# Performance work log

Measured on AMD Instinct MI355X. Metric: run time of the kernel, lower is better.

## Reference

```python
import jax, jax.numpy as jnp
import numpy as np

N_HEADS = 16
D_EMBED = 1024
N_CROSS = 768
D_HEAD = D_EMBED // N_HEADS


def setup_inputs() -> dict:
    key = jax.random.key(0)
    ks = jax.random.split(key, 10)
    B, S = 2, 2048
    x = jax.random.normal(ks[0], (B, S, D_EMBED), dtype=jnp.float32)
    context = jax.random.normal(ks[1], (B, S, N_CROSS), dtype=jnp.float32)
    sq = 1.0 / np.sqrt(D_EMBED)
    sc = 1.0 / np.sqrt(N_CROSS)
    Wq = jax.random.normal(ks[2], (D_EMBED, D_EMBED), dtype=jnp.float32) * sq
    bq = jnp.zeros((D_EMBED,), dtype=jnp.float32)
    Wk = jax.random.normal(ks[3], (N_CROSS, D_EMBED), dtype=jnp.float32) * sc
    bk = jnp.zeros((D_EMBED,), dtype=jnp.float32)
    Wv = jax.random.normal(ks[4], (N_CROSS, D_EMBED), dtype=jnp.float32) * sc
    bv = jnp.zeros((D_EMBED,), dtype=jnp.float32)
    Wo = jax.random.normal(ks[5], (D_EMBED, D_EMBED), dtype=jnp.float32) * sq
    bo = jnp.zeros((D_EMBED,), dtype=jnp.float32)
    return {"x": x, "context": context, "Wq": Wq, "bq": bq, "Wk": Wk, "bk": bk,
            "Wv": Wv, "bv": bv, "Wo": Wo, "bo": bo}


def reference(x, context, Wq, bq, Wk, bk, Wv, bv, Wo, bo):
    B, S, _ = x.shape

    def split_heads(t):  # [B,S,E] -> [B,H,S,Dh]
        return t.reshape(B, S, N_HEADS, D_HEAD).transpose(0, 2, 1, 3)

    q = split_heads(x @ Wq + bq)
    k = split_heads(context @ Wk + bk)
    v = split_heads(context @ Wv + bv)

    scale = 1.0 / np.sqrt(D_HEAD)
    scores = jnp.einsum('bhqd,bhkd->bhqk', q, k) * scale
    attn = jax.nn.softmax(scores, axis=-1)
    out = jnp.einsum('bhqk,bhkd->bhqd', attn, v)
    out = out.transpose(0, 2, 1, 3).reshape(B, S, D_EMBED)
    return out @ Wo + bo
```

## Files before the change

kernel.cpp:

```cpp
#include <hip/hip_runtime.h>
#include <math.h>


namespace {

typedef short bfr __attribute__((ext_vector_type(8)));
typedef short s4v __attribute__((ext_vector_type(4)));
typedef unsigned u4v __attribute__((ext_vector_type(4)));
typedef float accf __attribute__((ext_vector_type(16)));

#define MFMA32(a, b, c) __builtin_amdgcn_mfma_f32_32x32x16_bf16(a, b, c, 0, 0, 0)

__device__ inline short f2bf(float f) {
    unsigned u = __float_as_uint(f);
    u += 0x7fffu + ((u >> 16) & 1u);
    return (short)(u >> 16);
}
__device__ inline float bf2f(short s) {
    return __uint_as_float(((unsigned)(unsigned short)s) << 16);
}
__device__ inline float fexp2(float x) { return __builtin_amdgcn_exp2f(x); }
__device__ inline accf zero16() {
    accf z;
#pragma unroll
    for (int i = 0; i < 16; ++i) z[i] = 0.f;
    return z;
}
__device__ inline void dma16(const void* g, void* l) {
    __builtin_amdgcn_global_load_lds(
        (const __attribute__((address_space(1))) void*)g,
        (__attribute__((address_space(3))) void*)l, 16, 0, 0);
}

__global__ __launch_bounds__(256) void prep(
    const float* __restrict__ x, const float* __restrict__ ctx,
    short* __restrict__ xb, short* __restrict__ cb,
    const float* __restrict__ Wq, const float* __restrict__ Wk,
    const float* __restrict__ Wv, const float* __restrict__ Wo,
    short* __restrict__ Wqt, short* __restrict__ Wkt,
    short* __restrict__ Wvt, short* __restrict__ Wot) {
    __shared__ short t[64][68];
    const int bx = blockIdx.x;
    if (bx < 7168) {
        int i = bx * 256 + threadIdx.x;
        if (i < 1048576) {
            float4 v = ((const float4*)x)[i];
            s4v p = {f2bf(v.x), f2bf(v.y), f2bf(v.z), f2bf(v.w)};
            ((s4v*)xb)[i] = p;
        } else {
            int j = i - 1048576;
            float4 v = ((const float4*)ctx)[j];
            s4v p = {f2bf(v.x), f2bf(v.y), f2bf(v.z), f2bf(v.w)};
            ((s4v*)cb)[j] = p;
        }
        return;
    }
    const int idx = bx - 7168;
    const int z = idx >> 8, gy = (idx >> 4) & 15, gx = idx & 15;
    const float* W;
    short* Wt;
    int K;
    switch (z) {
        case 0: W = Wq; Wt = Wqt; K = 1024; break;
        case 1: W = Wk; Wt = Wkt; K = 768; break;
        case 2: W = Wv; Wt = Wvt; K = 768; break;
        default: W = Wo; Wt = Wot; K = 1024; break;
    }
    const int k0 = gy * 64;
    if (k0 >= K) return;
    const int tid = threadIdx.x;
    const int n0 = gx * 64;
    const int kr = tid >> 4, nc = (tid & 15) * 4;
#pragma unroll
    for (int rep = 0; rep < 4; ++rep) {
        int k = kr + rep * 16;
        float4 v = *(const float4*)&W[(size_t)(k0 + k) * 1024 + n0 + nc];
        t[nc + 0][k] = f2bf(v.x);
        t[nc + 1][k] = f2bf(v.y);
        t[nc + 2][k] = f2bf(v.z);
        t[nc + 3][k] = f2bf(v.w);
    }
    __syncthreads();
    const int nr = tid >> 4, kc = (tid & 15) * 4;
#pragma unroll
    for (int rep = 0; rep < 4; ++rep) {
        int n = nr + rep * 16;
        s4v p = {t[n][kc], t[n][kc + 1], t[n][kc + 2], t[n][kc + 3]};
        *(s4v*)&Wt[(size_t)(n0 + n) * K + k0 + kc] = p;
    }
}

__global__ __launch_bounds__(512, 6) void gemm_qkv(
    const short* __restrict__ xb, const short* __restrict__ cb,
    const short* __restrict__ Wqt, const short* __restrict__ Wkt,
    const short* __restrict__ Wvt, const float* __restrict__ bq,
    const float* __restrict__ bk, const float* __restrict__ bv,
    short* __restrict__ Qf, short* __restrict__ Kf, short* __restrict__ Vt,
    float qscale) {
    const int bid = blockIdx.x;
    const int z = bid >> 8;
    const int local = bid & 255;
    const short* A  = (z == 0) ? xb : cb;
    const short* Bt = (z == 0) ? Wqt : ((z == 1) ? Wkt : Wvt);
    const float* bias = (z == 0) ? bq : ((z == 1) ? bk : bv);
    const int K = (z == 0) ? 1024 : 768;
    const int NIT = K / 32;
    const float scale = (z == 0) ? qscale : 1.f;
    short* out = (z == 0) ? Qf : ((z == 1) ? Kf : Vt);

    __shared__ short As[12288];
    __shared__ short Bs[12288];
    const int t = threadIdx.x, lane = t & 63, w = t >> 6;
    const int lm = lane & 31, h2 = lane >> 5;
    const int wm = w & 1, wn = w >> 1;
    const int m0 = (local & 31) * 128, n0 = (local >> 5) * 128;

    const int st = t ^ ((t >> 3) & 7);
    const int srow = st >> 2, scol = (st & 3) * 8;
    const short* ga = A + (size_t)(m0 + srow) * K + scol;
    const short* gb = Bt + (size_t)(n0 + srow) * K + scol;

    const int xorv = (lm >> 1) & 7;
    const int rA0 = wm * 64 + lm, rB0 = wn * 32 + lm;

    accf acc[2] = {zero16(), zero16()};

    dma16(ga, &As[w * 512]);
    dma16(gb, &Bs[w * 512]);
    __builtin_amdgcn_sched_barrier(0);
    dma16(ga + 32, &As[4096 + w * 512]);
    dma16(gb + 32, &Bs[4096 + w * 512]);
    __builtin_amdgcn_sched_barrier(0);

    int buf = 0;
#pragma unroll 1
    for (int it = 0; it < NIT; ++it) {
        __builtin_amdgcn_sched_barrier(0);
        asm volatile("s_waitcnt vmcnt(2)" ::: "memory");
        __builtin_amdgcn_s_barrier();
        __builtin_amdgcn_sched_barrier(0);
        {
            const int nx = (it + 2 >= NIT) ? (it + 2 - NIT) : (it + 2);
            const int nb = (buf + 2 >= 3) ? (buf - 1) : (buf + 2);
            dma16(ga + nx * 32, &As[nb * 4096 + w * 512]);
            dma16(gb + nx * 32, &Bs[nb * 4096 + w * 512]);
        }
        const short* bA = &As[buf * 4096];
        const short* bB = &Bs[buf * 4096];
#pragma unroll
        for (int kk8 = 0; kk8 < 4; kk8 += 2) {
            bfr a0 = *(const bfr*)&bA[((rA0 * 4 + h2 + kk8) ^ xorv) * 8];
            bfr a1 = *(const bfr*)&bA[(((rA0 + 32) * 4 + h2 + kk8) ^ xorv) * 8];
            bfr b0 = *(const bfr*)&bB[((rB0 * 4 + h2 + kk8) ^ xorv) * 8];
            acc[0] = MFMA32(a0, b0, acc[0]);
            acc[1] = MFMA32(a1, b0, acc[1]);
        }
        buf = (buf + 1 == 3) ? 0 : buf + 1;
    }
    asm volatile("s_waitcnt vmcnt(0)" ::: "memory");
    __builtin_amdgcn_sched_barrier(0);

    const int n = n0 + wn * 32 + lm;
    const float bn = bias[n];
    const int hh = n >> 6, dd = n & 63;
#pragma unroll
    for (int mt = 0; mt < 2; ++mt) {
        const int mbase = m0 + wm * 64 + mt * 32 + 4 * h2;
        if (z != 2) {
            const int cb2 = (dd >> 4) * 512 + ((dd >> 3) & 1) * 256 + (dd & 7);
#pragma unroll
            for (int r = 0; r < 16; ++r) {
                const int m = mbase + (r & 3) + 8 * (r >> 2);
                const int bb = m >> 11, q = m & 2047;
                float v = (acc[mt][r] + bn) * scale;
                out[((size_t)((bb * 16 + hh) * 64 + (q >> 5))) * 2048 +
                    cb2 + (q & 31) * 8] = f2bf(v);
            }
        } else {
            const int dblk = dd >> 5, lmv = dd & 31;
#pragma unroll
            for (int g = 0; g < 4; ++g) {
                const int m = mbase + 8 * g;
                const int bb = m >> 11, s = m & 2047;
                const int kvt = s >> 6, kc = (s >> 4) & 3;
                const int h2v = (s >> 3) & 1, j0 = s & 7;
                s4v pq = {f2bf(acc[mt][4 * g + 0] + bn),
                          f2bf(acc[mt][4 * g + 1] + bn),
                          f2bf(acc[mt][4 * g + 2] + bn),
                          f2bf(acc[mt][4 * g + 3] + bn)};
                *(s4v*)(out +
                        ((size_t)(((bb * 16 + hh) * 32 + kvt) * 2 + dblk)) * 2048 +
                        kc * 512 + h2v * 256 + lmv * 8 + j0) = pq;
            }
        }
    }
}

__global__ __launch_bounds__(512, 6) void gemm_o(
    const short* __restrict__ Af, const short* __restrict__ Bt,
    const float* __restrict__ bias, float* __restrict__ out) {
    constexpr int K = 1024, NIT = 32;
    __shared__ short As[12288];
    __shared__ short Bs[6144];
    const int t = threadIdx.x, lane = t & 63, w = t >> 6;
    const int lm = lane & 31, h2 = lane >> 5;
    const int wm = w & 3, wn = w >> 2;
    const int bid = blockIdx.x;
    const int m0 = (bid & 31) * 128, n0 = (bid >> 5) * 64;

    const int st = t ^ ((t >> 3) & 7);
    const int srow = st >> 2, scol = (st & 3) * 8;
    const short* ga = Af + (size_t)(m0 + srow) * K + scol;
    const short* gb = Bt + (size_t)(n0 + srow) * K + scol;
    const bool bw = (w < 4);

    const int xorv = (lm >> 1) & 7;
    const int rA0 = wm * 32 + lm, rB0 = wn * 32 + lm;

    accf acc = zero16();

    dma16(ga, &As[w * 512]);
    if (bw) dma16(gb, &Bs[w * 512]);
    __builtin_amdgcn_sched_barrier(0);
    dma16(ga + 32, &As[4096 + w * 512]);
    if (bw) dma16(gb + 32, &Bs[2048 + w * 512]);
    __builtin_amdgcn_sched_barrier(0);

    int buf = 0;
#pragma unroll 1
    for (int it = 0; it < NIT; ++it) {
        __builtin_amdgcn_sched_barrier(0);
        if (bw) {
            asm volatile("s_waitcnt vmcnt(2)" ::: "memory");
        } else {
            asm volatile("s_waitcnt vmcnt(1)" ::: "memory");
        }
        __builtin_amdgcn_s_barrier();
        __builtin_amdgcn_sched_barrier(0);
        {
            const int nx = (it + 2 >= NIT) ? (it + 2 - NIT) : (it + 2);
            const int nb = (buf + 2 >= 3) ? (buf - 1) : (buf + 2);
            dma16(ga + nx * 32, &As[nb * 4096 + w * 512]);
            if (bw) dma16(gb + nx * 32, &Bs[nb * 2048 + w * 512]);
        }
        const short* bA = &As[buf * 4096];
        const short* bB = &Bs[buf * 2048];
#pragma unroll
        for (int kk8 = 0; kk8 < 4; kk8 += 2) {
            bfr a0 = *(const bfr*)&bA[((rA0 * 4 + h2 + kk8) ^ xorv) * 8];
            bfr b0 = *(const bfr*)&bB[((rB0 * 4 + h2 + kk8) ^ xorv) * 8];
            acc = MFMA32(a0, b0, acc);
        }
        buf = (buf + 1 == 3) ? 0 : buf + 1;
    }
    asm volatile("s_waitcnt vmcnt(0)" ::: "memory");
    __builtin_amdgcn_sched_barrier(0);

    const int n = n0 + wn * 32 + lm;
    const float bn = bias[n];
    const int mbase = m0 + wm * 32 + 4 * h2;
#pragma unroll
    for (int r = 0; r < 16; ++r) {
        const int m = mbase + (r & 3) + 8 * (r >> 2);
        out[(size_t)m * 1024 + n] = acc[r] + bn;
    }
}

__global__ __launch_bounds__(256, 3) void attn(
    const short* __restrict__ Qf, const short* __restrict__ Kf,
    const short* __restrict__ Vt, short* __restrict__ part) {
    __shared__ short smem[16384];
    const int bid = blockIdx.x;
    const int hidx = bid & 31, qb = bid >> 5;
    const int b = hidx >> 4, h = hidx & 15;
    const int lane = threadIdx.x & 63, wv = threadIdx.x >> 6;
    const int lm = lane & 31, h2 = lane >> 5;
    const bool hb = h2 != 0;
    const int q0 = qb * 128 + wv * 32;

    const short* qbase =
        Qf + ((size_t)(hidx * 64 + (q0 >> 5))) * 2048 + lane * 8;
    bfr qf[4];
#pragma unroll
    for (int kc = 0; kc < 4; ++kc) qf[kc] = *(const bfr*)(qbase + kc * 512);

    const short* khead = Kf + (size_t)hidx * 131072;
    const short* vhead = Vt + (size_t)hidx * 131072;
    const short* gsrc =
        ((wv < 2) ? (khead + wv * 2048) : (vhead + (wv - 2) * 2048)) + lane * 8;

#pragma unroll
    for (int i = 0; i < 4; ++i)
        dma16(gsrc + i * 512, &smem[wv * 2048 + i * 512]);

    accf oa0 = zero16(), oa1 = zero16();
    float la0 = 0.f, la1 = 0.f;

#pragma unroll 1
    for (int it = 0; it < 32; ++it) {
        const int p = it & 1;
        __syncthreads();
        if (it + 1 < 32) {
            const short* gn = gsrc + (size_t)(it + 1) * 4096;
            short* ln = &smem[(1 - p) * 8192 + wv * 2048];
#pragma unroll
            for (int i = 0; i < 4; ++i) dma16(gn + i * 512, ln + i * 512);
        }
        const short* kb = &smem[p * 8192];
        bfr kf0[4], kf1[4], vf0[4], vf1[4];
#pragma unroll
        for (int kc = 0; kc < 4; ++kc) {
            kf0[kc] = *(const bfr*)&kb[kc * 512 + lane * 8];
            kf1[kc] = *(const bfr*)&kb[2048 + kc * 512 + lane * 8];
            vf0[kc] = *(const bfr*)&kb[4096 + kc * 512 + lane * 8];
            vf1[kc] = *(const bfr*)&kb[6144 + kc * 512 + lane * 8];
        }
        accf s0 = zero16(), s1 = zero16();
#pragma unroll
        for (int kc = 0; kc < 4; ++kc) {
            s0 = MFMA32(kf0[kc], qf[kc], s0);
            s1 = MFMA32(kf1[kc], qf[kc], s1);
        }

#pragma unroll
        for (int i = 0; i < 16; ++i) s0[i] = fexp2(s0[i]);
#pragma unroll
        for (int i = 0; i < 16; ++i) s1[i] = fexp2(s1[i]);
#pragma unroll
        for (int i = 0; i < 16; ++i) {
            if (i & 1) la1 += s0[i] + s1[i];
            else       la0 += s0[i] + s1[i];
        }

        bfr pb[4];
#pragma unroll
        for (int kc = 0; kc < 4; ++kc) {
            const accf& s = (kc < 2) ? s0 : s1;
            const int base = 8 * (kc & 1);
            unsigned Lw0 = __builtin_amdgcn_perm(__float_as_uint(s[base + 1]),
                                                 __float_as_uint(s[base + 0]),
                                                 0x07060302u);
            unsigned Lw1 = __builtin_amdgcn_perm(__float_as_uint(s[base + 3]),
                                                 __float_as_uint(s[base + 2]),
                                                 0x07060302u);
            unsigned Hw0 = __builtin_amdgcn_perm(__float_as_uint(s[base + 5]),
                                                 __float_as_uint(s[base + 4]),
                                                 0x07060302u);
            unsigned Hw1 = __builtin_amdgcn_perm(__float_as_uint(s[base + 7]),
                                                 __float_as_uint(s[base + 6]),
                                                 0x07060302u);
            unsigned c0 = hb ? Lw0 : Hw0;
            unsigned c1 = hb ? Lw1 : Hw1;
            unsigned r0 = (unsigned)__shfl_xor((int)c0, 32);
            unsigned r1 = (unsigned)__shfl_xor((int)c1, 32);
            u4v pw = {hb ? r0 : Lw0, hb ? r1 : Lw1,
                      hb ? Hw0 : r0, hb ? Hw1 : r1};
            pb[kc] = __builtin_bit_cast(bfr, pw);
        }

#pragma unroll
        for (int kc = 0; kc < 4; ++kc) {
            oa0 = MFMA32(vf0[kc], pb[kc], oa0);
            oa1 = MFMA32(vf1[kc], pb[kc], oa1);
        }
    }

    float ls = la0 + la1;
    ls += __shfl_xor(ls, 32);
    const float iv = 1.f / ls;

    short* orow = part + (size_t)(b * 2048 + q0 + lm) * 1024 + h * 64;
#pragma unroll
    for (int dt = 0; dt < 2; ++dt) {
        const accf& oa = dt ? oa1 : oa0;
#pragma unroll
        for (int g = 0; g < 4; ++g) {
            const int d0 = dt * 32 + 4 * h2 + 8 * g;
            s4v p = {f2bf(oa[4 * g + 0] * iv), f2bf(oa[4 * g + 1] * iv),
                     f2bf(oa[4 * g + 2] * iv), f2bf(oa[4 * g + 3] * iv)};
            *(s4v*)(orow + d0) = p;
        }
    }
}

}

extern "C" void kernel_launch(void* const* d_in, const int* in_sizes, int n_in,
                              void* d_out, int out_size, void* d_ws,
                              size_t ws_size, hipStream_t stream) {
    const float* x   = (const float*)d_in[0];
    const float* ctx = (const float*)d_in[1];
    const float* Wq  = (const float*)d_in[2];
    const float* bq  = (const float*)d_in[3];
    const float* Wk  = (const float*)d_in[4];
    const float* bk  = (const float*)d_in[5];
    const float* Wv  = (const float*)d_in[6];
    const float* bv  = (const float*)d_in[7];
    const float* Wo  = (const float*)d_in[8];
    const float* bo  = (const float*)d_in[9];

    short* xb  = (short*)d_ws;
    short* cb  = xb + (size_t)4096 * 1024;
    short* Wqt = cb + (size_t)4096 * 768;
    short* Wkt = Wqt + (size_t)1024 * 1024;
    short* Wvt = Wkt + (size_t)1024 * 768;
    short* Wot = Wvt + (size_t)1024 * 768;
    short* Qf  = Wot + (size_t)1024 * 1024;
    short* Kf  = Qf + (size_t)4096 * 1024;
    short* Vt  = Kf + (size_t)4096 * 1024;
    short* p0  = Vt + (size_t)4096 * 1024;

    prep<<<8192, 256, 0, stream>>>(x, ctx, xb, cb, Wq, Wk, Wv, Wo,
                                   Wqt, Wkt, Wvt, Wot);

    const float qscale = 0.125f * 1.44269504088896f;
    gemm_qkv<<<768, 512, 0, stream>>>(xb, cb, Wqt, Wkt, Wvt,
                                      bq, bk, bv, Qf, Kf, Vt, qscale);

    attn<<<512, 256, 0, stream>>>(Qf, Kf, Vt, p0);

    gemm_o<<<512, 512, 0, stream>>>(p0, Wot, bo, (float*)d_out);
}
```

Measured before the change: 199.3 us.

## Process two query tiles per wave in attention to reuse K/V fragments

The attention kernel now runs 2 waves per block instead of 4, and each wave handles 64 query rows (two 32-row tiles) rather than 32. Each K and V fragment loaded from LDS is reused for two MFMAs, which halves LDS reads per unit of compute and the number of waves sharing each tile. Each wave also issues twice as many DMA loads to stage K/V. The cost is roughly double the accumulator and score registers per wave, and dropping the occupancy hint from launch bounds, which may lower occupancy and latency hiding.

```diff
diff --git a/kernel.cpp b/kernel.cpp
--- a/kernel.cpp
+++ b/kernel.cpp
@@ -266,35 +266,39 @@
     }
 }
 
-__global__ __launch_bounds__(256, 3) void attn(
+__global__ __launch_bounds__(128) void attn(
     const short* __restrict__ Qf, const short* __restrict__ Kf,
     const short* __restrict__ Vt, short* __restrict__ part) {
     __shared__ short smem[16384];
     const int bid = blockIdx.x;
-    const int hidx = bid & 31, qb = bid >> 5;
+    const int hidx = bid & 31, qg = bid >> 5;
     const int b = hidx >> 4, h = hidx & 15;
     const int lane = threadIdx.x & 63, wv = threadIdx.x >> 6;
     const int lm = lane & 31, h2 = lane >> 5;
     const bool hb = h2 != 0;
-    const int q0 = qb * 128 + wv * 32;
+    const int q0 = qg * 128 + wv * 64;
 
     const short* qbase =
         Qf + ((size_t)(hidx * 64 + (q0 >> 5))) * 2048 + lane * 8;
-    bfr qf[4];
-#pragma unroll
-    for (int kc = 0; kc < 4; ++kc) qf[kc] = *(const bfr*)(qbase + kc * 512);
+    bfr qfA[4], qfB[4];
+#pragma unroll
+    for (int kc = 0; kc < 4; ++kc) {
+        qfA[kc] = *(const bfr*)(qbase + kc * 512);
+        qfB[kc] = *(const bfr*)(qbase + 2048 + kc * 512);
+    }
 
     const short* khead = Kf + (size_t)hidx * 131072;
     const short* vhead = Vt + (size_t)hidx * 131072;
-    const short* gsrc =
-        ((wv < 2) ? (khead + wv * 2048) : (vhead + (wv - 2) * 2048)) + lane * 8;
-
-#pragma unroll
-    for (int i = 0; i < 4; ++i)
-        dma16(gsrc + i * 512, &smem[wv * 2048 + i * 512]);
-
-    accf oa0 = zero16(), oa1 = zero16();
-    float la0 = 0.f, la1 = 0.f;
+    const short* gsrc = ((wv == 0) ? khead : vhead) + lane * 8;
+    const int ldst = wv * 4096;
+
+#pragma unroll
+    for (int i = 0; i < 8; ++i)
+        dma16(gsrc + i * 512, &smem[ldst + i * 512]);
+
+    accf oaA0 = zero16(), oaA1 = zero16();
+    accf oaB0 = zero16(), oaB1 = zero16();
+    float laA0 = 0.f, laA1 = 0.f, laB0 = 0.f, laB1 = 0.f;
 
 #pragma unroll 1
     for (int it = 0; it < 32; ++it) {
@@ -302,40 +306,45 @@
         __syncthreads();
         if (it + 1 < 32) {
             const short* gn = gsrc + (size_t)(it + 1) * 4096;
-            short* ln = &smem[(1 - p) * 8192 + wv * 2048];
-#pragma unroll
-            for (int i = 0; i < 4; ++i) dma16(gn + i * 512, ln + i * 512);
+            short* ln = &smem[(1 - p) * 8192 + ldst];
+#pragma unroll
+            for (int i = 0; i < 8; ++i) dma16(gn + i * 512, ln + i * 512);
         }
         const short* kb = &smem[p * 8192];
-        bfr kf0[4], kf1[4], vf0[4], vf1[4];
+        bfr kf0[4], kf1[4];
 #pragma unroll
         for (int kc = 0; kc < 4; ++kc) {
             kf0[kc] = *(const bfr*)&kb[kc * 512 + lane * 8];
             kf1[kc] = *(const bfr*)&kb[2048 + kc * 512 + lane * 8];
-            vf0[kc] = *(const bfr*)&kb[4096 + kc * 512 + lane * 8];
-            vf1[kc] = *(const bfr*)&kb[6144 + kc * 512 + lane * 8];
-        }
-        accf s0 = zero16(), s1 = zero16();
-#pragma unroll
-        for (int kc = 0; kc < 4; ++kc) {
-            s0 = MFMA32(kf0[kc], qf[kc], s0);
-            s1 = MFMA32(kf1[kc], qf[kc], s1);
-        }
-
-#pragma unroll
-        for (int i = 0; i < 16; ++i) s0[i] = fexp2(s0[i]);
-#pragma unroll
-        for (int i = 0; i < 16; ++i) s1[i] = fexp2(s1[i]);
+        }
+        accf sA0 = zero16(), sA1 = zero16();
+        accf sB0 = zero16(), sB1 = zero16();
+#pragma unroll
+        for (int kc = 0; kc < 4; ++kc) {
+            sA0 = MFMA32(kf0[kc], qfA[kc], sA0);
+            sA1 = MFMA32(kf1[kc], qfA[kc], sA1);
+            sB0 = MFMA32(kf0[kc], qfB[kc], sB0);
+            sB1 = MFMA32(kf1[kc], qfB[kc], sB1);
+        }
+
+#pragma unroll
+        for (int i = 0; i < 16; ++i) sA0[i] = fexp2(sA0[i]);
+#pragma unroll
+        for (int i = 0; i < 16; ++i) sA1[i] = fexp2(sA1[i]);
+#pragma unroll
+        for (int i = 0; i < 16; ++i) sB0[i] = fexp2(sB0[i]);
+#pragma unroll
+        for (int i = 0; i < 16; ++i) sB1[i] = fexp2(sB1[i]);
 #pragma unroll
         for (int i = 0; i < 16; ++i) {
-            if (i & 1) la1 += s0[i] + s1[i];
-            else       la0 += s0[i] + s1[i];
-        }
-
-        bfr pb[4];
-#pragma unroll
-        for (int kc = 0; kc < 4; ++kc) {
-            const accf& s = (kc < 2) ? s0 : s1;
+            if (i & 1) { laA1 += sA0[i] + sA1[i]; laB1 += sB0[i] + sB1[i]; }
+            else       { laA0 += sA0[i] + sA1[i]; laB0 += sB0[i] + sB1[i]; }
+        }
+
+        bfr pbA[4], pbB[4];
+#pragma unroll
+        for (int kc = 0; kc < 4; ++kc) {
+            const accf& s = (kc < 2) ? sA0 : sA1;
             const int base = 8 * (kc & 1);
             unsigned Lw0 = __builtin_amdgcn_perm(__float_as_uint(s[base + 1]),
                                                  __float_as_uint(s[base + 0]),
@@ -355,30 +364,77 @@
             unsigned r1 = (unsigned)__shfl_xor((int)c1, 32);
             u4v pw = {hb ? r0 : Lw0, hb ? r1 : Lw1,
                       hb ? Hw0 : r0, hb ? Hw1 : r1};
-            pb[kc] = __builtin_bit_cast(bfr, pw);
-        }
-
-#pragma unroll
-        for (int kc = 0; kc < 4; ++kc) {
-            oa0 = MFMA32(vf0[kc], pb[kc], oa0);
-            oa1 = MFMA32(vf1[kc], pb[kc], oa1);
-        }
-    }
-
-    float ls = la0 + la1;
-    ls += __shfl_xor(ls, 32);
-    const float iv = 1.f / ls;
-
-    short* orow = part + (size_t)(b * 2048 + q0 + lm) * 1024 + h * 64;
+            pbA[kc] = __builtin_bit_cast(bfr, pw);
+        }
+#pragma unroll
+        for (int kc = 0; kc < 4; ++kc) {
+            const accf& s = (kc < 2) ? sB0 : sB1;
+            const int base = 8 * (kc & 1);
+            unsigned Lw0 = __builtin_amdgcn_perm(__float_as_uint(s[base + 1]),
+                                                 __float_as_uint(s[base + 0]),
+                                                 0x07060302u);
+            unsigned Lw1 = __builtin_amdgcn_perm(__float_as_uint(s[base + 3]),
+                                                 __float_as_uint(s[base + 2]),
+                                                 0x07060302u);
+            unsigned Hw0 = __builtin_amdgcn_perm(__float_as_uint(s[base + 5]),
+                                                 __float_as_uint(s[base + 4]),
+                                                 0x07060302u);
+            unsigned Hw1 = __builtin_amdgcn_perm(__float_as_uint(s[base + 7]),
+                                                 __float_as_uint(s[base + 6]),
+                                                 0x07060302u);
+            unsigned c0 = hb ? Lw0 : Hw0;
+            unsigned c1 = hb ? Lw1 : Hw1;
+            unsigned r0 = (unsigned)__shfl_xor((int)c0, 32);
+            unsigned r1 = (unsigned)__shfl_xor((int)c1, 32);
+            u4v pw = {hb ? r0 : Lw0, hb ? r1 : Lw1,
+                      hb ? Hw0 : r0, hb ? Hw1 : r1};
+            pbB[kc] = __builtin_bit_cast(bfr, pw);
+        }
+
+        bfr vf0[4], vf1[4];
+#pragma unroll
+        for (int kc = 0; kc < 4; ++kc) {
+            vf0[kc] = *(const bfr*)&kb[4096 + kc * 512 + lane * 8];
+            vf1[kc] = *(const bfr*)&kb[6144 + kc * 512 + lane * 8];
+        }
+#pragma unroll
+        for (int kc = 0; kc < 4; ++kc) {
+            oaA0 = MFMA32(vf0[kc], pbA[kc], oaA0);
+            oaA1 = MFMA32(vf1[kc], pbA[kc], oaA1);
+            oaB0 = MFMA32(vf0[kc], pbB[kc], oaB0);
+            oaB1 = MFMA32(vf1[kc], pbB[kc], oaB1);
+        }
+    }
+
+    float lsA = laA0 + laA1;
+    lsA += __shfl_xor(lsA, 32);
+    const float ivA = 1.f / lsA;
+    float lsB = laB0 + laB1;
+    lsB += __shfl_xor(lsB, 32);
+    const float ivB = 1.f / lsB;
+
+    short* orowA = part + (size_t)(b * 2048 + q0 + lm) * 1024 + h * 64;
+    short* orowB = orowA + (size_t)32 * 1024;
 #pragma unroll
     for (int dt = 0; dt < 2; ++dt) {
-        const accf& oa = dt ? oa1 : oa0;
+        const accf& oa = dt ? oaA1 : oaA0;
 #pragma unroll
         for (int g = 0; g < 4; ++g) {
             const int d0 = dt * 32 + 4 * h2 + 8 * g;
-            s4v p = {f2bf(oa[4 * g + 0] * iv), f2bf(oa[4 * g + 1] * iv),
-                     f2bf(oa[4 * g + 2] * iv), f2bf(oa[4 * g + 3] * iv)};
-            *(s4v*)(orow + d0) = p;
+            s4v p = {f2bf(oa[4 * g + 0] * ivA), f2bf(oa[4 * g + 1] * ivA),
+                     f2bf(oa[4 * g + 2] * ivA), f2bf(oa[4 * g + 3] * ivA)};
+            *(s4v*)(orowA + d0) = p;
+        }
+    }
+#pragma unroll
+    for (int dt = 0; dt < 2; ++dt) {
+        const accf& oa = dt ? oaB1 : oaB0;
+#pragma unroll
+        for (int g = 0; g < 4; ++g) {
+            const int d0 = dt * 32 + 4 * h2 + 8 * g;
+            s4v p = {f2bf(oa[4 * g + 0] * ivB), f2bf(oa[4 * g + 1] * ivB),
+                     f2bf(oa[4 * g + 2] * ivB), f2bf(oa[4 * g + 3] * ivB)};
+            *(s4v*)(orowB + d0) = p;
         }
     }
 }
@@ -417,7 +473,7 @@
     gemm_qkv<<<768, 512, 0, stream>>>(xb, cb, Wqt, Wkt, Wvt,
                                       bq, bk, bv, Qf, Kf, Vt, qscale);
 
-    attn<<<512, 256, 0, stream>>>(Qf, Kf, Vt, p0);
+    attn<<<512, 128, 0, stream>>>(Qf, Kf, Vt, p0);
 
     gemm_o<<<512, 512, 0, stream>>>(p0, Wot, bo, (float*)d_out);
 }
```

Result: slower. 224.5 us (+12.7%).

## Load K/V fragments directly from global memory instead of LDS double buffer

Applied to the files above, without the earlier changes.

The attention kernel no longer stages K and V tiles through a double-buffered shared-memory ring filled by async DMA with a per-iteration __syncthreads. Each wave now reads its K/V MFMA fragments straight from global memory, relying on L2/cache reuse across the four waves. This removes the barriers and LDS traffic and drops the occupancy hint from the launch bounds. It gives up explicit prefetch overlap and makes each wave fetch the full K/V tile redundantly from global memory.

```diff
diff --git a/kernel.cpp b/kernel.cpp
--- a/kernel.cpp
+++ b/kernel.cpp
@@ -266,10 +266,9 @@
     }
 }
 
-__global__ __launch_bounds__(256, 3) void attn(
+__global__ __launch_bounds__(256) void attn(
     const short* __restrict__ Qf, const short* __restrict__ Kf,
     const short* __restrict__ Vt, short* __restrict__ part) {
-    __shared__ short smem[16384];
     const int bid = blockIdx.x;
     const int hidx = bid & 31, qb = bid >> 5;
     const int b = hidx >> 4, h = hidx & 15;
@@ -284,36 +283,23 @@
 #pragma unroll
     for (int kc = 0; kc < 4; ++kc) qf[kc] = *(const bfr*)(qbase + kc * 512);
 
-    const short* khead = Kf + (size_t)hidx * 131072;
-    const short* vhead = Vt + (size_t)hidx * 131072;
-    const short* gsrc =
-        ((wv < 2) ? (khead + wv * 2048) : (vhead + (wv - 2) * 2048)) + lane * 8;
-
-#pragma unroll
-    for (int i = 0; i < 4; ++i)
-        dma16(gsrc + i * 512, &smem[wv * 2048 + i * 512]);
+    const short* khead = Kf + (size_t)hidx * 131072 + lane * 8;
+    const short* vhead = Vt + (size_t)hidx * 131072 + lane * 8;
 
     accf oa0 = zero16(), oa1 = zero16();
     float la0 = 0.f, la1 = 0.f;
 
 #pragma unroll 1
     for (int it = 0; it < 32; ++it) {
-        const int p = it & 1;
-        __syncthreads();
-        if (it + 1 < 32) {
-            const short* gn = gsrc + (size_t)(it + 1) * 4096;
-            short* ln = &smem[(1 - p) * 8192 + wv * 2048];
-#pragma unroll
-            for (int i = 0; i < 4; ++i) dma16(gn + i * 512, ln + i * 512);
-        }
-        const short* kb = &smem[p * 8192];
+        const short* kit = khead + (size_t)it * 4096;
+        const short* vit = vhead + (size_t)it * 4096;
         bfr kf0[4], kf1[4], vf0[4], vf1[4];
 #pragma unroll
         for (int kc = 0; kc < 4; ++kc) {
-            kf0[kc] = *(const bfr*)&kb[kc * 512 + lane * 8];
-            kf1[kc] = *(const bfr*)&kb[2048 + kc * 512 + lane * 8];
-            vf0[kc] = *(const bfr*)&kb[4096 + kc * 512 + lane * 8];
-            vf1[kc] = *(const bfr*)&kb[6144 + kc * 512 + lane * 8];
+            kf0[kc] = *(const bfr*)(kit + kc * 512);
+            kf1[kc] = *(const bfr*)(kit + 2048 + kc * 512);
+            vf0[kc] = *(const bfr*)(vit + kc * 512);
+            vf1[kc] = *(const bfr*)(vit + 2048 + kc * 512);
         }
         accf s0 = zero16(), s1 = zero16();
 #pragma unroll
```

Result: no change. 202.4 us (+1.5%).
